# Kernel tuning notes

Measured on AMD Instinct MI355X. Metric: run time of the kernel, lower is better.

## Reference

```python
import jax, jax.numpy as jnp
import numpy as np
from jax.scipy.linalg import cholesky, solve_triangular

SIGMA2 = 0.001   # likelihood.variance (fixed in source)
JITTER = 1e-5


def hankel(v, L):
    # Direct windowed gather; math-identical to the one-hot matmul in the source.
    Nv, Dv = v.shape
    idx = jnp.arange(Nv - L + 1)[:, None] + jnp.arange(L)[None, :]  # [Nv-L+1, L]
    return v[idx].reshape(Nv - L + 1, L * Dv)


def _sqdist(A, B):
    # ||a-b||^2, clipped for numerical safety
    d = jnp.sum(A * A, 1)[:, None] + jnp.sum(B * B, 1)[None, :] - 2.0 * A @ B.T
    return jnp.maximum(d, 0.0)


def _psi_stats(Z, Xmu, Xvar, l2, variance):
    # RBF (ARD) expected-kernel statistics (GPflow conventions).
    N = Xmu.shape[0]
    # psi0: E[k(x,x)] = variance per point, summed over N
    psi0 = jnp.asarray(N, Xmu.dtype) * variance
    # psi1[n,m] = var * prod_q (1+s/l2)^-1/2 * exp(-0.5 (mu-z)^2/(l2+s))
    denom = l2 + Xvar                                        # [N,D]
    logdet1 = -0.5 * jnp.sum(jnp.log1p(Xvar / l2), axis=1)   # [N]
    quad1 = -0.5 * jnp.sum((Xmu[:, None, :] - Z[None, :, :]) ** 2 / denom[:, None, :], axis=2)  # [N,M]
    psi1 = variance * jnp.exp(logdet1[:, None] + quad1)      # [N,M]
    # psi2[n,m,k] = var^2 * prod_q (1+2s/l2)^-1/2
    #   * exp(-(zm-zk)^2/(4 l2) - (mu - (zm+zk)/2)^2 / (2s + l2))
    a = 1.0 / (2.0 * Xvar + l2)                              # [N,D]
    cn = variance ** 2 * jnp.exp(-0.5 * jnp.sum(jnp.log1p(2.0 * Xvar / l2), axis=1))  # [N]
    Zs = Z / (2.0 * jnp.sqrt(l2))
    dZ2 = _sqdist(Zs, Zs)                                    # [M,M], (zm-zk)^2/(4 l2)
    # expand (mu - zbar)^2 * a  without a [N,M,M,D] tensor
    T1 = jnp.sum(a * Xmu * Xmu, axis=1)                      # [N]
    T2 = (a * Xmu) @ Z.T                                     # [N,M]
    T3 = a @ (Z * Z).T                                       # [N,M]
    T4 = jnp.einsum('nq,mq,kq->nmk', a, Z, Z)                # [N,M,M]
    quad2 = (T1[:, None, None] - T2[:, :, None] - T2[:, None, :]
             + 0.25 * (T3[:, :, None] + T3[:, None, :]) + 0.5 * T4)  # [N,M,M]
    psi2 = jnp.sum(cn[:, None, None] * jnp.exp(-dZ2[None, :, :] - quad2), axis=0)  # [M,M]
    return psi0, psi1, psi2


def build_likelihood(X_mean, X_var, Z, lengthscales, variance, Lt):
    N_tot, Q = X_mean.shape
    M = Z.shape[0]
    N = N_tot - Lt
    sigma2 = jnp.asarray(SIGMA2, X_mean.dtype)
    sigma = jnp.sqrt(sigma2)
    l2 = lengthscales ** 2

    X_m = hankel(X_mean[:N_tot - 1], Lt)   # [N, Lt*Q]
    X_v = hankel(X_var[:N_tot - 1], Lt)
    X_mo, X_vo = X_mean[Lt:], X_var[Lt:]   # [N, Q]
    X_mb, X_vb = X_mean[:Lt], X_var[:Lt]   # [Lt, Q]

    Kuu = variance * jnp.exp(-0.5 * _sqdist(Z / lengthscales, Z / lengthscales)) \
          + JITTER * jnp.eye(M, dtype=X_mean.dtype)
    psi0, psi1, psi2 = _psi_stats(Z, X_m, X_v, l2, variance)

    L = cholesky(Kuu, lower=True)
    A = solve_triangular(L, psi1.T, lower=True) / sigma            # [M,N]
    tmp = solve_triangular(L, psi2, lower=True)
    AAT = solve_triangular(L, tmp.T, lower=True) / sigma2          # [M,M]
    B = AAT + jnp.eye(M, dtype=X_mean.dtype)
    LB = cholesky(B, lower=True)
    log_det_B = 2.0 * jnp.sum(jnp.log(jnp.diag(LB)))
    c = solve_triangular(LB, A @ X_mo, lower=True) / sigma         # [M,Q]

    NQ = jnp.asarray(N * Q, X_mean.dtype)
    two_pi = jnp.asarray(2.0 * np.pi, X_mean.dtype)
    ent = 0.5 * jnp.sum(jnp.log(X_vo)) + 0.5 * NQ * jnp.log(two_pi)
    ent2 = -jnp.asarray(Lt * Q, X_mean.dtype) * jnp.log(two_pi) \
           - 0.5 * jnp.sum(X_mb ** 2 + X_vb)

    bound = -0.5 * NQ * jnp.log(two_pi * sigma2)
    bound += -0.5 / sigma2 * (jnp.sum(X_vo) + jnp.sum(X_mo ** 2))
    bound += -0.5 * Q * (psi0 / sigma2 - jnp.trace(AAT))
    bound += -0.5 * Q * log_det_B
    bound += 0.5 * jnp.sum(c ** 2)
    bound += ent + ent2
    return bound


def setup_inputs() -> dict:
    key = jax.random.key(0)
    k1, k2, k3 = jax.random.split(key, 3)
    N, Q, Lt, M = 4096, 4, 8, 128
    D = Lt * Q
    X_mean = jax.random.normal(k1, (N + Lt, Q), dtype=jnp.float32)
    X_var = jax.random.uniform(k2, (N + Lt, Q), dtype=jnp.float32, minval=0.1, maxval=1.0)
    Z = jax.random.normal(k3, (M, D), dtype=jnp.float32)
    lengthscales = 2.0 * jnp.ones((D,), dtype=jnp.float32)
    variance = jnp.asarray(1.0, dtype=jnp.float32)
    return {"X_mean": X_mean, "X_var": X_var, "Z": Z,
            "lengthscales": lengthscales, "variance": variance, "Lt": Lt}


def reference(X_mean, X_var, Z, lengthscales, variance, Lt):
    return build_likelihood(X_mean, X_var, Z, lengthscales, variance, Lt)
```

## Files before the change

kernel.cpp:

```cpp
#include <hip/hip_runtime.h>

#define NN   4096
#define NQ   (NN*4)
#define QQ   4
#define LTT  8
#define DD   32
#define MM   128
#define SIG2 0.001f
#define JIT  1e-5f
#define LOG2E 1.4426950408889634f

typedef _Float16 half8 __attribute__((ext_vector_type(8)));
typedef float    f32x4 __attribute__((ext_vector_type(4)));

__device__ __forceinline__ float fexp2(float x) { return exp2f(x); }

__device__ __forceinline__ float rlane(float v, int l) {
    return __uint_as_float(__builtin_amdgcn_readlane(__float_as_uint(v), l));
}

__global__ __launch_bounds__(256) void prepstatic_kernel(
    const float* __restrict__ Xm, const float* __restrict__ Xv,
    const float* __restrict__ Zg, const float* __restrict__ ls,
    const float* __restrict__ varp,
    float4* __restrict__ pk4, _Float16* __restrict__ bh,
    float* __restrict__ L1p, float* __restrict__ bbp, float* __restrict__ sumsP,
    float* __restrict__ Kuu, float* __restrict__ sp, _Float16* __restrict__ Zh,
    float* __restrict__ Yg, float* __restrict__ scalars, int* __restrict__ cnt)
{
    int b = blockIdx.x, tid = threadIdx.x;
    if (b < 16) {
        __shared__ float ra[256], rb[256], rc[256];
        int n = b*256 + tid;
        float var = varp[0];
        float slog2 = 0.f, slog1 = 0.f, T1 = 0.f, c0 = 0.f;
        #pragma unroll 8
        for (int q = 0; q < DD; ++q) {
            float xm = Xm[n*QQ + q];
            float xv = Xv[n*QQ + q];
            float l  = ls[q];
            float l2 = l*l;
            float a    = 1.0f / (2.0f*xv + l2);
            float dinv = 1.0f / (l2 + xv);
            float4 v;
            v.x = LOG2E * a * xm;
            v.y = LOG2E * (-0.25f * a);
            v.z = dinv;
            v.w = -2.0f * dinv * xm;
            pk4[n*DD + q] = v;
            bh[n*DD + q] = (_Float16)(0.5f * LOG2E * (1.0f/l2 - a));
            slog2 += log1pf(2.0f*xv/l2);
            slog1 += log1pf(xv/l2);
            T1    += a*xm*xm;
            c0    += dinv*xm*xm;
        }
        L1p[n] = 0.5f * LOG2E * (2.0f*logf(var) - 0.5f*slog2 - T1);
        bbp[n] = logf(var) - 0.5f*slog1 - 0.5f*c0;
        float s1 = 0.f, s2 = 0.f, s3 = 0.f;
        #pragma unroll
        for (int c = 0; c < QQ; ++c) {
            float mo = Xm[(n+LTT)*QQ + c];
            float vo = Xv[(n+LTT)*QQ + c];
            s1 += vo + mo*mo;
            s2 += logf(vo);
        }
        if (n < LTT) {
            #pragma unroll
            for (int c = 0; c < QQ; ++c) {
                float mb = Xm[n*QQ+c], vb = Xv[n*QQ+c];
                s3 += mb*mb + vb;
            }
        }
        ra[tid]=s1; rb[tid]=s2; rc[tid]=s3;
        __syncthreads();
        for (int s = 128; s; s >>= 1) {
            if (tid < s) { ra[tid]+=ra[tid+s]; rb[tid]+=rb[tid+s]; rc[tid]+=rc[tid+s]; }
            __syncthreads();
        }
        if (tid == 0) { sumsP[b*3+0]=ra[0]; sumsP[b*3+1]=rb[0]; sumsP[b*3+2]=rc[0]; }
    } else if (b < 80) {
        int idx = (b-16)*256 + tid;
        int i = idx >> 7, j = idx & 127;
        float var = varp[0];
        float s = 0.f;
        for (int q = 0; q < DD; ++q) {
            float l = ls[q];
            float d = (Zg[i*DD+q] - Zg[j*DD+q]) / l;
            s += d*d;
        }
        float v = var * __expf(-0.5f*s);
        if (i == j) v += JIT;
        Kuu[idx] = v;
    } else {
        if (tid < MM) {
            float s = 0.f;
            for (int q = 0; q < DD; ++q) {
                float l = ls[q]; float z = Zg[tid*DD+q];
                s += z*z / (4.0f*l*l);
            }
            sp[tid] = LOG2E * s;
        }
        for (int e = tid; e < MM*DD; e += 256) Zh[e] = (_Float16)Zg[e];
        for (int e = tid; e < 512; e += 256) Yg[e] = 0.f;
        if (tid < 8) scalars[tid] = 0.f;
        if (tid == 0) *cnt = 0;
    }
}

__device__ __forceinline__ void dev_chol(float* mat, int tid)
{
    int wv = tid >> 6, ln = tid & 63;
    for (int p = 0; p < 8; ++p) {
        int base = p*16;
        if (wv == 0) {
            int r0 = base + ln, r1 = r0 + 64;
            bool h0 = r0 < 128, h1 = r1 < 128;
            float a0[16], a1[16];
            #pragma unroll
            for (int c = 0; c < 16; ++c) {
                a0[c] = h0 ? mat[r0*132 + base + c] : 0.f;
                a1[c] = h1 ? mat[r1*132 + base + c] : 0.f;
            }
            #pragma unroll
            for (int kk = 0; kk < 16; ++kk) {
                float d   = rlane(a0[kk], kk);
                float rdk = rsqrtf(d);
                float sq  = d * rdk;
                a0[kk] = (ln == kk) ? sq : a0[kk] * rdk;
                a1[kk] *= rdk;
                #pragma unroll
                for (int j = kk+1; j < 16; ++j) {
                    float ljv = rlane(a0[kk], j);
                    a0[j] = fmaf(-a0[kk], ljv, a0[j]);
                    a1[j] = fmaf(-a1[kk], ljv, a1[j]);
                }
            }
            #pragma unroll
            for (int c = 0; c < 16; ++c) {
                if (h0) mat[r0*132 + base + c] = a0[c];
                if (h1) mat[r1*132 + base + c] = a1[c];
            }
        }
        __syncthreads();
        int S = 112 - base;
        if (S > 0) {
            int T = S >> 2, nb = base + 16;
            int nT = (T*(T+1)) >> 1;
            for (int t = tid; t < nT; t += 256) {
                int ti = (int)(0.5f*(sqrtf(8.f*(float)t + 1.f) - 1.f));
                if ((ti+1)*(ti+2)/2 <= t) ++ti;
                else if (ti*(ti+1)/2 > t) --ti;
                int tj = t - ((ti*(ti+1))>>1);
                int i0 = nb + ti*4, j0 = nb + tj*4;
                float ac[4][4];
                #pragma unroll
                for (int r = 0; r < 4; ++r)
                    #pragma unroll
                    for (int s = 0; s < 4; ++s) ac[r][s] = mat[(i0+r)*132 + j0 + s];
                #pragma unroll
                for (int c4 = 0; c4 < 4; ++c4) {
                    float4 av[4], bv[4];
                    #pragma unroll
                    for (int r = 0; r < 4; ++r) {
                        av[r] = *(const float4*)&mat[(i0+r)*132 + base + c4*4];
                        bv[r] = *(const float4*)&mat[(j0+r)*132 + base + c4*4];
                    }
                    #pragma unroll
                    for (int r = 0; r < 4; ++r)
                        #pragma unroll
                        for (int s = 0; s < 4; ++s)
                            ac[r][s] -= av[r].x*bv[s].x + av[r].y*bv[s].y
                                      + av[r].z*bv[s].z + av[r].w*bv[s].w;
                }
                #pragma unroll
                for (int r = 0; r < 4; ++r)
                    #pragma unroll
                    for (int s = 0; s < 4; ++s) mat[(i0+r)*132 + j0 + s] = ac[r][s];
            }
        }
        __syncthreads();
    }
}

__device__ __forceinline__ void dev_dinv(const float* mat, float* dinvb, int tid)
{
    int wv = tid >> 6, ln = tid & 63;
    if (ln < 16) {
        int c = ln;
        for (int bd = wv; bd < 8; bd += 4) {
            int base = bd*16;
            float x[16];
            #pragma unroll
            for (int i = 0; i < 16; ++i) {
                float dii = mat[(base+i)*132 + base + i];
                float s = 0.f;
                #pragma unroll
                for (int j = 0; j < i; ++j) s += mat[(base+i)*132 + base + j] * x[j];
                float v;
                if (i < c) v = 0.f;
                else if (i == c) v = 1.0f / dii;
                else v = -s / dii;
                x[i] = v;
            }
            #pragma unroll
            for (int i = 0; i < 16; ++i) dinvb[bd*256 + i*16 + c] = x[i];
        }
    }
    __syncthreads();
}

template<int C>
__device__ __forceinline__ void dev_solve(const float* mat, const float* dinvb,
                                          float* tmp, float* rhs, int tid)
{
    const int AT = 16*C;
    int r = tid / C, cc = tid % C;
    for (int bi = 0; bi < 8; ++bi) {
        float acc = 0.f;
        if (tid < AT) {
            acc = rhs[(bi*16+r)*C + cc];
            for (int bk = 0; bk < bi; ++bk) {
                #pragma unroll
                for (int kk = 0; kk < 16; ++kk)
                    acc -= mat[(bi*16+r)*132 + bk*16+kk] * rhs[(bk*16+kk)*C + cc];
            }
        }
        __syncthreads();
        if (tid < AT) tmp[r*C + cc] = acc;
        __syncthreads();
        if (tid < AT) {
            float w = 0.f;
            #pragma unroll
            for (int kk = 0; kk < 16; ++kk)
                w += dinvb[bi*256 + r*16 + kk] * tmp[kk*C + cc];
            rhs[(bi*16+r)*C + cc] = w;
        }
        __syncthreads();
    }
}

template<int C>
__device__ __forceinline__ void dev_bsolve(const float* mat, const float* dinvb,
                                           float* tmp, float* rhs, int tid)
{
    const int AT = 16*C;
    int r = tid / C, cc = tid % C;
    for (int bi = 7; bi >= 0; --bi) {
        float acc = 0.f;
        if (tid < AT) {
            acc = rhs[(bi*16+r)*C + cc];
            for (int bj = bi+1; bj < 8; ++bj) {
                #pragma unroll
                for (int kk = 0; kk < 16; ++kk)
                    acc -= mat[(bj*16+kk)*132 + bi*16 + r] * rhs[(bj*16+kk)*C + cc];
            }
        }
        __syncthreads();
        if (tid < AT) tmp[r*C + cc] = acc;
        __syncthreads();
        if (tid < AT) {
            float w = 0.f;
            #pragma unroll
            for (int kk = 0; kk < 16; ++kk)
                w += dinvb[bi*256 + kk*16 + r] * tmp[kk*C + cc];
            rhs[(bi*16+r)*C + cc] = w;
        }
        __syncthreads();
    }
}

__global__ __launch_bounds__(256) void k1chol_kernel(
    const float* __restrict__ Xm, const float* __restrict__ Zg,
    const float4* __restrict__ pk4, const float* __restrict__ L1p,
    const float* __restrict__ bbp, const float* __restrict__ sp,
    float* __restrict__ r_g, float* __restrict__ Yg, float* __restrict__ psi2,
    const float* __restrict__ Kuu, float* __restrict__ Lg,
    float* __restrict__ Dinvg, float* __restrict__ scalars)
{
    __shared__ float shm[19200];
    int tid = threadIdx.x;
    if (blockIdx.x < 256) {
        float* Zl    = shm;
        float* yredl = shm + 4224;
        { int e = blockIdx.x*64 + tid; if (tid < 64) psi2[e] = 0.f; }
        for (int e = tid; e < MM*DD; e += 256)
            Zl[(e>>5)*33 + (e&31)] = Zg[e];
        __syncthreads();
        int m = tid & 127, half = tid >> 7;
        float zr[DD];
        #pragma unroll
        for (int q = 0; q < DD; ++q) zr[q] = Zl[m*33 + q];
        float sm = sp[m];
        float y0=0.f, y1=0.f, y2=0.f, y3=0.f;
        int n0 = blockIdx.x*16 + half*8;
        for (int i = 0; i < 8; ++i) {
            int n = n0 + i;
            float L1n = L1p[n], bbn = bbp[n];
            const float4* pkn = pk4 + n*DD;
            float racc = 0.f, q1 = 0.f;
            #pragma unroll
            for (int q = 0; q < DD; ++q) {
                float4 v = pkn[q];
                float z = zr[q];
                racc = fmaf(v.x, z, racc);
                racc = fmaf(v.y, z*z, racc);
                float t = fmaf(v.z, z, v.w);
                q1 = fmaf(t, z, q1);
            }
            r_g[n*MM + m] = L1n + racc - sm;
            float p1 = __expf(fmaf(-0.5f, q1, bbn));
            float4 xo = *(const float4*)(Xm + (LTT+n)*QQ);
            y0 = fmaf(p1, xo.x, y0); y1 = fmaf(p1, xo.y, y1);
            y2 = fmaf(p1, xo.z, y2); y3 = fmaf(p1, xo.w, y3);
        }
        if (half == 0) {
            yredl[m*4+0]=y0; yredl[m*4+1]=y1; yredl[m*4+2]=y2; yredl[m*4+3]=y3;
        }
        __syncthreads();
        if (half == 1) {
            yredl[m*4+0]+=y0; yredl[m*4+1]+=y1; yredl[m*4+2]+=y2; yredl[m*4+3]+=y3;
        }
        __syncthreads();
        for (int e = tid; e < 512; e += 256) atomicAdd(&Yg[e], yredl[e]);
    } else {
        float* mat   = shm;
        float* dinvb = shm + 16896;
        float* red   = shm + 18944;
        for (int e = tid; e < 16384; e += 256) mat[(e>>7)*132 + (e&127)] = Kuu[e];
        __syncthreads();
        dev_chol(mat, tid);
        float ld = (tid < 128) ? logf(mat[tid*132 + tid]) : 0.f;
        red[tid] = ld; __syncthreads();
        for (int s = 128; s; s >>= 1) { if (tid < s) red[tid] += red[tid+s]; __syncthreads(); }
        if (tid == 0) scalars[0] = red[0];
        dev_dinv(mat, dinvb, tid);
        for (int e = tid; e < 16384; e += 256) Lg[e] = mat[(e>>7)*132 + (e&127)];
        for (int e = tid; e < 2048; e += 256) Dinvg[e] = dinvb[e];
    }
}

__global__ __launch_bounds__(256) void psi2_kernel(
    const _Float16* __restrict__ Zh, const float* __restrict__ r_g,
    const _Float16* __restrict__ bh, float* __restrict__ psi2)
{
    __shared__ float pacc[4][64][4];
    int tid = threadIdx.x;
    int w = tid >> 6, l = tid & 63, lm = l & 15, lg = l >> 4;
    int b = blockIdx.x;
    int nq = b / 36, t = b - nq*36;
    int kt = (int)(0.5f*(sqrtf(8.f*(float)t + 1.f) - 1.f));
    if ((kt+1)*(kt+2)/2 <= t) ++kt;
    else if (kt*(kt+1)/2 > t) --kt;
    int mt = t - ((kt*(kt+1))>>1);

    half8 Bf = ((const half8*)Zh)[(kt*16 + lm)*4 + lg];
    half8 Zm = ((const half8*)Zh)[(mt*16 + lm)*4 + lg];
    f32x4 z4; z4[0]=0.f; z4[1]=0.f; z4[2]=0.f; z4[3]=0.f;
    f32x4 acc0 = z4, acc1 = z4;
    int n0g = nq*128 + w*32;
    const float* rbase = r_g + (size_t)n0g*MM;
    const half8* bbase = (const half8*)bh + (size_t)n0g*4;
    for (int i = 0; i < 32; i += 2) {
        half8 bf0 = bbase[i*4 + lg];
        half8 bf1 = bbase[i*4 + 4 + lg];
        const float* rn0 = rbase + i*MM;
        f32x4 rm0 = *(const f32x4*)(rn0 + mt*16 + lg*4);
        f32x4 rm1 = *(const f32x4*)(rn0 + MM + mt*16 + lg*4);
        float rk0 = rn0[kt*16 + lm];
        float rk1 = rn0[MM + kt*16 + lm];
        half8 A0 = Zm * bf0;
        half8 A1 = Zm * bf1;
        f32x4 p0 = __builtin_amdgcn_mfma_f32_16x16x32_f16(A0, Bf, z4, 0, 0, 0);
        f32x4 p1 = __builtin_amdgcn_mfma_f32_16x16x32_f16(A1, Bf, z4, 0, 0, 0);
        acc0[0] += fexp2(p0[0] + rm0[0] + rk0);
        acc0[1] += fexp2(p0[1] + rm0[1] + rk0);
        acc0[2] += fexp2(p0[2] + rm0[2] + rk0);
        acc0[3] += fexp2(p0[3] + rm0[3] + rk0);
        acc1[0] += fexp2(p1[0] + rm1[0] + rk1);
        acc1[1] += fexp2(p1[1] + rm1[1] + rk1);
        acc1[2] += fexp2(p1[2] + rm1[2] + rk1);
        acc1[3] += fexp2(p1[3] + rm1[3] + rk1);
    }
    f32x4 acc;
    acc[0]=acc0[0]+acc1[0]; acc[1]=acc0[1]+acc1[1];
    acc[2]=acc0[2]+acc1[2]; acc[3]=acc0[3]+acc1[3];
    #pragma unroll
    for (int j = 0; j < 4; ++j) pacc[w][l][j] = acc[j];
    __syncthreads();
    {
        int ll = tid >> 2, j = tid & 3;
        float s = pacc[0][ll][j] + pacc[1][ll][j] + pacc[2][ll][j] + pacc[3][ll][j];
        int row = mt*16 + (ll >> 4)*4 + j;
        int col = kt*16 + (ll & 15);
        atomicAdd(&psi2[row*MM + col], s);
        if (mt != kt) atomicAdd(&psi2[col*MM + row], s);
    }
}

__global__ __launch_bounds__(256) void cholG_kernel(
    const float* __restrict__ Kuu, const float* __restrict__ psi2,
    const float* __restrict__ Yg, const float* __restrict__ Lg,
    const float* __restrict__ Dinvg, const float* __restrict__ varp,
    const float* __restrict__ sumsP,
    float* __restrict__ scalars, int* __restrict__ cnt, float* __restrict__ out)
{
    __shared__ float mat[128*132];
    __shared__ float dinvb[8*256];
    __shared__ float rhs[128*8];
    __shared__ float tmp[128];
    __shared__ float red[256];
    int tid = threadIdx.x;
    if (blockIdx.x == 0) {
        for (int e = tid; e < 16384; e += 256)
            mat[(e>>7)*132 + (e&127)] = Kuu[e] + (1.0f/SIG2)*psi2[e];
        __syncthreads();
        dev_chol(mat, tid);
        float ld = (tid < 128) ? logf(mat[tid*132 + tid]) : 0.f;
        red[tid] = ld; __syncthreads();
        for (int s = 128; s; s >>= 1) { if (tid < s) red[tid] += red[tid+s]; __syncthreads(); }
        if (tid == 0) scalars[1] = red[0];
        dev_dinv(mat, dinvb, tid);
        if (tid < 256) { rhs[tid] = Yg[tid]; rhs[tid+256] = Yg[tid+256]; }
        __syncthreads();
        dev_solve<4>(mat, dinvb, tmp, rhs, tid);
        float c2 = rhs[tid]*rhs[tid] + rhs[tid+256]*rhs[tid+256];
        red[tid] = c2; __syncthreads();
        for (int s = 128; s; s >>= 1) { if (tid < s) red[tid] += red[tid+s]; __syncthreads(); }
        if (tid == 0) scalars[2] = red[0];
    } else {
        int c0 = (blockIdx.x - 1) * 8;
        for (int e = tid; e < 16384; e += 256) mat[(e>>7)*132 + (e&127)] = Lg[e];
        for (int e = tid; e < 2048; e += 256) dinvb[e] = Dinvg[e];
        for (int e = tid; e < 1024; e += 256) {
            int i = e >> 3, cc = e & 7;
            rhs[e] = (i == c0 + cc) ? 1.0f : 0.0f;
        }
        __syncthreads();
        dev_bsolve<8>(mat, dinvb, tmp, rhs, tid);
        int i = tid & 127, cp = tid >> 7;
        float vv0=0.f, vv1=0.f, vv2=0.f, vv3=0.f;
        for (int j = 0; j < 128; ++j) {
            float pj = psi2[j*MM + i];
            vv0 = fmaf(pj, rhs[j*8 + cp*4 + 0], vv0);
            vv1 = fmaf(pj, rhs[j*8 + cp*4 + 1], vv1);
            vv2 = fmaf(pj, rhs[j*8 + cp*4 + 2], vv2);
            vv3 = fmaf(pj, rhs[j*8 + cp*4 + 3], vv3);
        }
        float part = rhs[i*8 + cp*4 + 0]*vv0 + rhs[i*8 + cp*4 + 1]*vv1
                   + rhs[i*8 + cp*4 + 2]*vv2 + rhs[i*8 + cp*4 + 3]*vv3;
        red[tid] = part; __syncthreads();
        for (int s = 128; s; s >>= 1) { if (tid < s) red[tid] += red[tid+s]; __syncthreads(); }
        if (tid == 0) atomicAdd(&scalars[3], red[0]);
    }
    if (tid == 0) {
        __threadfence();
        int old = atomicAdd(cnt, 1);
        if (old == 16) {
            float ldK  = scalars[0];
            float ldG  = atomicAdd(&scalars[1], 0.0f);
            float c2s  = atomicAdd(&scalars[2], 0.0f);
            float trr  = atomicAdd(&scalars[3], 0.0f);
            float s1=0.f, s2=0.f, s3=0.f;
            for (int b2 = 0; b2 < 16; ++b2) {
                s1 += sumsP[b2*3+0]; s2 += sumsP[b2*3+1]; s3 += sumsP[b2*3+2];
            }
            float var = varp[0];
            float trAAT   = trr / SIG2;
            float logdetB = 2.0f * (ldG - ldK);
            float sumc2   = c2s / (SIG2*SIG2);
            float psi0    = (float)NN * var;
            const float LOG2PI = 1.837877066409345f;
            float NQf = (float)NQ;
            float bound = -0.5f*NQf*(LOG2PI + logf(SIG2));
            bound += -0.5f/SIG2 * s1;
            bound += -0.5f*(float)QQ*(psi0/SIG2 - trAAT);
            bound += -0.5f*(float)QQ*logdetB;
            bound += 0.5f*sumc2;
            bound += 0.5f*s2 + 0.5f*NQf*LOG2PI;
            bound += -(float)(LTT*QQ)*LOG2PI - 0.5f*s3;
            out[0] = bound;
        }
    }
}

extern "C" void kernel_launch(void* const* d_in, const int* in_sizes, int n_in,
                              void* d_out, int out_size, void* d_ws, size_t ws_size,
                              hipStream_t stream)
{
    (void)in_sizes; (void)n_in; (void)out_size; (void)ws_size;
    const float* Xm   = (const float*)d_in[0];
    const float* Xv   = (const float*)d_in[1];
    const float* Zg   = (const float*)d_in[2];
    const float* ls   = (const float*)d_in[3];
    const float* varp = (const float*)d_in[4];

    float* p = (float*)d_ws;
    float4*   pk4   = (float4*)p;       p += NN*DD*4;
    float*    r_g   = p;                p += NN*MM;
    _Float16* bh    = (_Float16*)p;     p += NN*DD/2;
    _Float16* Zh    = (_Float16*)p;     p += MM*DD/2;
    float*    L1p   = p;                p += NN;
    float*    bbp   = p;                p += NN;
    float*    sp    = p;                p += MM;
    float*    Kuu   = p;                p += MM*MM;
    float*    Lg    = p;                p += MM*MM;
    float*    Dinvg = p;                p += 2048;
    float*    psi2  = p;                p += MM*MM;
    float*    Yg    = p;                p += 512;
    float*    sumsP = p;                p += 64;
    float*    scalars = p;              p += 8;
    int*      cnt   = (int*)p;          p += 4;

    prepstatic_kernel<<<81, 256, 0, stream>>>(Xm, Xv, Zg, ls, varp,
                                              pk4, bh, L1p, bbp, sumsP, Kuu, sp, Zh,
                                              Yg, scalars, cnt);
    k1chol_kernel<<<257, 256, 0, stream>>>(Xm, Zg, pk4, L1p, bbp, sp, r_g, Yg, psi2,
                                           Kuu, Lg, Dinvg, scalars);
    psi2_kernel<<<1152, 256, 0, stream>>>(Zh, r_g, bh, psi2);
    cholG_kernel<<<17, 256, 0, stream>>>(Kuu, psi2, Yg, Lg, Dinvg, varp, sumsP,
                                         scalars, cnt, (float*)d_out);
}
```

Baseline: 187.6 us.

## Move Kuu Cholesky into psi2 launch and widen serial solver blocks to 512 threads

```diff
diff --git a/kernel.cpp b/kernel.cpp
--- a/kernel.cpp
+++ b/kernel.cpp
@@ -107,6 +107,58 @@
     }
 }
 
+__global__ __launch_bounds__(256) void k1_kernel(
+    const float* __restrict__ Xm, const float* __restrict__ Zg,
+    const float4* __restrict__ pk4, const float* __restrict__ L1p,
+    const float* __restrict__ bbp, const float* __restrict__ sp,
+    float* __restrict__ r_g, float* __restrict__ Yg, float* __restrict__ psi2)
+{
+    __shared__ float Zl[MM*33];
+    __shared__ float yredl[MM*QQ];
+    int tid = threadIdx.x;
+    { int e = blockIdx.x*64 + tid; if (tid < 64) psi2[e] = 0.f; }
+    for (int e = tid; e < MM*DD; e += 256)
+        Zl[(e>>5)*33 + (e&31)] = Zg[e];
+    __syncthreads();
+    int m = tid & 127, half = tid >> 7;
+    float zr[DD];
+    #pragma unroll
+    for (int q = 0; q < DD; ++q) zr[q] = Zl[m*33 + q];
+    float sm = sp[m];
+    float y0=0.f, y1=0.f, y2=0.f, y3=0.f;
+    int n0 = blockIdx.x*16 + half*8;
+    for (int i = 0; i < 8; ++i) {
+        int n = n0 + i;
+        float L1n = L1p[n], bbn = bbp[n];
+        const float4* pkn = pk4 + n*DD;
+        float racc = 0.f, q1 = 0.f;
+        #pragma unroll
+        for (int q = 0; q < DD; ++q) {
+            float4 v = pkn[q];
+            float z = zr[q];
+            racc = fmaf(v.x, z, racc);
+            racc = fmaf(v.y, z*z, racc);
+            float t = fmaf(v.z, z, v.w);
+            q1 = fmaf(t, z, q1);
+        }
+        r_g[n*MM + m] = L1n + racc - sm;
+        float p1 = __expf(fmaf(-0.5f, q1, bbn));
+        float4 xo = *(const float4*)(Xm + (LTT+n)*QQ);
+        y0 = fmaf(p1, xo.x, y0); y1 = fmaf(p1, xo.y, y1);
+        y2 = fmaf(p1, xo.z, y2); y3 = fmaf(p1, xo.w, y3);
+    }
+    if (half == 0) {
+        yredl[m*4+0]=y0; yredl[m*4+1]=y1; yredl[m*4+2]=y2; yredl[m*4+3]=y3;
+    }
+    __syncthreads();
+    if (half == 1) {
+        yredl[m*4+0]+=y0; yredl[m*4+1]+=y1; yredl[m*4+2]+=y2; yredl[m*4+3]+=y3;
+    }
+    __syncthreads();
+    for (int e = tid; e < 512; e += 256) atomicAdd(&Yg[e], yredl[e]);
+}
+
+template<int NT>
 __device__ __forceinline__ void dev_chol(float* mat, int tid)
 {
     int wv = tid >> 6, ln = tid & 63;
@@ -146,7 +198,7 @@
         if (S > 0) {
             int T = S >> 2, nb = base + 16;
             int nT = (T*(T+1)) >> 1;
-            for (int t = tid; t < nT; t += 256) {
+            for (int t = tid; t < nT; t += NT) {
                 int ti = (int)(0.5f*(sqrtf(8.f*(float)t + 1.f) - 1.f));
                 if ((ti+1)*(ti+2)/2 <= t) ++ti;
                 else if (ti*(ti+1)/2 > t) --ti;
@@ -182,12 +234,13 @@
     }
 }
 
+template<int NT>
 __device__ __forceinline__ void dev_dinv(const float* mat, float* dinvb, int tid)
 {
     int wv = tid >> 6, ln = tid & 63;
     if (ln < 16) {
         int c = ln;
-        for (int bd = wv; bd < 8; bd += 4) {
+        for (int bd = wv; bd < 8; bd += NT/64) {
             int base = bd*16;
             float x[16];
             #pragma unroll
@@ -207,36 +260,6 @@
         }
     }
     __syncthreads();
-}
-
-template<int C>
-__device__ __forceinline__ void dev_solve(const float* mat, const float* dinvb,
-                                          float* tmp, float* rhs, int tid)
-{
-    const int AT = 16*C;
-    int r = tid / C, cc = tid % C;
-    for (int bi = 0; bi < 8; ++bi) {
-        float acc = 0.f;
-        if (tid < AT) {
-            acc = rhs[(bi*16+r)*C + cc];
-            for (int bk = 0; bk < bi; ++bk) {
-                #pragma unroll
-                for (int kk = 0; kk < 16; ++kk)
-                    acc -= mat[(bi*16+r)*132 + bk*16+kk] * rhs[(bk*16+kk)*C + cc];
-            }
-        }
-        __syncthreads();
-        if (tid < AT) tmp[r*C + cc] = acc;
-        __syncthreads();
-        if (tid < AT) {
-            float w = 0.f;
-            #pragma unroll
-            for (int kk = 0; kk < 16; ++kk)
-                w += dinvb[bi*256 + r*16 + kk] * tmp[kk*C + cc];
-            rhs[(bi*16+r)*C + cc] = w;
-        }
-        __syncthreads();
-    }
 }
 
 template<int C>
@@ -269,135 +292,83 @@
     }
 }
 
-__global__ __launch_bounds__(256) void k1chol_kernel(
-    const float* __restrict__ Xm, const float* __restrict__ Zg,
-    const float4* __restrict__ pk4, const float* __restrict__ L1p,
-    const float* __restrict__ bbp, const float* __restrict__ sp,
-    float* __restrict__ r_g, float* __restrict__ Yg, float* __restrict__ psi2,
+__global__ __launch_bounds__(512) void psi2chol_kernel(
+    const _Float16* __restrict__ Zh, const float* __restrict__ r_g,
+    const _Float16* __restrict__ bh, float* __restrict__ psi2,
     const float* __restrict__ Kuu, float* __restrict__ Lg,
     float* __restrict__ Dinvg, float* __restrict__ scalars)
 {
-    __shared__ float shm[19200];
+    __shared__ float shm[19456];
     int tid = threadIdx.x;
-    if (blockIdx.x < 256) {
-        float* Zl    = shm;
-        float* yredl = shm + 4224;
-        { int e = blockIdx.x*64 + tid; if (tid < 64) psi2[e] = 0.f; }
-        for (int e = tid; e < MM*DD; e += 256)
-            Zl[(e>>5)*33 + (e&31)] = Zg[e];
-        __syncthreads();
-        int m = tid & 127, half = tid >> 7;
-        float zr[DD];
-        #pragma unroll
-        for (int q = 0; q < DD; ++q) zr[q] = Zl[m*33 + q];
-        float sm = sp[m];
-        float y0=0.f, y1=0.f, y2=0.f, y3=0.f;
-        int n0 = blockIdx.x*16 + half*8;
-        for (int i = 0; i < 8; ++i) {
-            int n = n0 + i;
-            float L1n = L1p[n], bbn = bbp[n];
-            const float4* pkn = pk4 + n*DD;
-            float racc = 0.f, q1 = 0.f;
-            #pragma unroll
-            for (int q = 0; q < DD; ++q) {
-                float4 v = pkn[q];
-                float z = zr[q];
-                racc = fmaf(v.x, z, racc);
-                racc = fmaf(v.y, z*z, racc);
-                float t = fmaf(v.z, z, v.w);
-                q1 = fmaf(t, z, q1);
-            }
-            r_g[n*MM + m] = L1n + racc - sm;
-            float p1 = __expf(fmaf(-0.5f, q1, bbn));
-            float4 xo = *(const float4*)(Xm + (LTT+n)*QQ);
-            y0 = fmaf(p1, xo.x, y0); y1 = fmaf(p1, xo.y, y1);
-            y2 = fmaf(p1, xo.z, y2); y3 = fmaf(p1, xo.w, y3);
-        }
-        if (half == 0) {
-            yredl[m*4+0]=y0; yredl[m*4+1]=y1; yredl[m*4+2]=y2; yredl[m*4+3]=y3;
-        }
-        __syncthreads();
-        if (half == 1) {
-            yredl[m*4+0]+=y0; yredl[m*4+1]+=y1; yredl[m*4+2]+=y2; yredl[m*4+3]+=y3;
-        }
-        __syncthreads();
-        for (int e = tid; e < 512; e += 256) atomicAdd(&Yg[e], yredl[e]);
-    } else {
+    if (blockIdx.x == 0) {
         float* mat   = shm;
         float* dinvb = shm + 16896;
         float* red   = shm + 18944;
-        for (int e = tid; e < 16384; e += 256) mat[(e>>7)*132 + (e&127)] = Kuu[e];
-        __syncthreads();
-        dev_chol(mat, tid);
-        float ld = (tid < 128) ? logf(mat[tid*132 + tid]) : 0.f;
-        red[tid] = ld; __syncthreads();
-        for (int s = 128; s; s >>= 1) { if (tid < s) red[tid] += red[tid+s]; __syncthreads(); }
+        for (int e = tid; e < 16384; e += 512) mat[(e>>7)*132 + (e&127)] = Kuu[e];
+        __syncthreads();
+        dev_chol<512>(mat, tid);
+        red[tid] = (tid < 128) ? logf(mat[tid*132 + tid]) : 0.f;
+        __syncthreads();
+        for (int s = 256; s; s >>= 1) { if (tid < s) red[tid] += red[tid+s]; __syncthreads(); }
         if (tid == 0) scalars[0] = red[0];
-        dev_dinv(mat, dinvb, tid);
-        for (int e = tid; e < 16384; e += 256) Lg[e] = mat[(e>>7)*132 + (e&127)];
-        for (int e = tid; e < 2048; e += 256) Dinvg[e] = dinvb[e];
-    }
-}
-
-__global__ __launch_bounds__(256) void psi2_kernel(
-    const _Float16* __restrict__ Zh, const float* __restrict__ r_g,
-    const _Float16* __restrict__ bh, float* __restrict__ psi2)
-{
-    __shared__ float pacc[4][64][4];
-    int tid = threadIdx.x;
-    int w = tid >> 6, l = tid & 63, lm = l & 15, lg = l >> 4;
-    int b = blockIdx.x;
-    int nq = b / 36, t = b - nq*36;
-    int kt = (int)(0.5f*(sqrtf(8.f*(float)t + 1.f) - 1.f));
-    if ((kt+1)*(kt+2)/2 <= t) ++kt;
-    else if (kt*(kt+1)/2 > t) --kt;
-    int mt = t - ((kt*(kt+1))>>1);
-
-    half8 Bf = ((const half8*)Zh)[(kt*16 + lm)*4 + lg];
-    half8 Zm = ((const half8*)Zh)[(mt*16 + lm)*4 + lg];
-    f32x4 z4; z4[0]=0.f; z4[1]=0.f; z4[2]=0.f; z4[3]=0.f;
-    f32x4 acc0 = z4, acc1 = z4;
-    int n0g = nq*128 + w*32;
-    const float* rbase = r_g + (size_t)n0g*MM;
-    const half8* bbase = (const half8*)bh + (size_t)n0g*4;
-    for (int i = 0; i < 32; i += 2) {
-        half8 bf0 = bbase[i*4 + lg];
-        half8 bf1 = bbase[i*4 + 4 + lg];
-        const float* rn0 = rbase + i*MM;
-        f32x4 rm0 = *(const f32x4*)(rn0 + mt*16 + lg*4);
-        f32x4 rm1 = *(const f32x4*)(rn0 + MM + mt*16 + lg*4);
-        float rk0 = rn0[kt*16 + lm];
-        float rk1 = rn0[MM + kt*16 + lm];
-        half8 A0 = Zm * bf0;
-        half8 A1 = Zm * bf1;
-        f32x4 p0 = __builtin_amdgcn_mfma_f32_16x16x32_f16(A0, Bf, z4, 0, 0, 0);
-        f32x4 p1 = __builtin_amdgcn_mfma_f32_16x16x32_f16(A1, Bf, z4, 0, 0, 0);
-        acc0[0] += fexp2(p0[0] + rm0[0] + rk0);
-        acc0[1] += fexp2(p0[1] + rm0[1] + rk0);
-        acc0[2] += fexp2(p0[2] + rm0[2] + rk0);
-        acc0[3] += fexp2(p0[3] + rm0[3] + rk0);
-        acc1[0] += fexp2(p1[0] + rm1[0] + rk1);
-        acc1[1] += fexp2(p1[1] + rm1[1] + rk1);
-        acc1[2] += fexp2(p1[2] + rm1[2] + rk1);
-        acc1[3] += fexp2(p1[3] + rm1[3] + rk1);
-    }
-    f32x4 acc;
-    acc[0]=acc0[0]+acc1[0]; acc[1]=acc0[1]+acc1[1];
-    acc[2]=acc0[2]+acc1[2]; acc[3]=acc0[3]+acc1[3];
-    #pragma unroll
-    for (int j = 0; j < 4; ++j) pacc[w][l][j] = acc[j];
-    __syncthreads();
-    {
-        int ll = tid >> 2, j = tid & 3;
-        float s = pacc[0][ll][j] + pacc[1][ll][j] + pacc[2][ll][j] + pacc[3][ll][j];
-        int row = mt*16 + (ll >> 4)*4 + j;
-        int col = kt*16 + (ll & 15);
-        atomicAdd(&psi2[row*MM + col], s);
-        if (mt != kt) atomicAdd(&psi2[col*MM + row], s);
-    }
-}
-
-__global__ __launch_bounds__(256) void cholG_kernel(
+        dev_dinv<512>(mat, dinvb, tid);
+        for (int e = tid; e < 16384; e += 512) Lg[e] = mat[(e>>7)*132 + (e&127)];
+        for (int e = tid; e < 2048; e += 512) Dinvg[e] = dinvb[e];
+    } else {
+        float (*pacc)[64][4] = (float(*)[64][4])shm;
+        int w = tid >> 6, l = tid & 63, lm = l & 15, lg = l >> 4;
+        int b = blockIdx.x - 1;
+        int t = b % 36, nq = b / 36;
+        int kt = (int)(0.5f*(sqrtf(8.f*(float)t + 1.f) - 1.f));
+        if ((kt+1)*(kt+2)/2 <= t) ++kt;
+        else if (kt*(kt+1)/2 > t) --kt;
+        int mt = t - ((kt*(kt+1))>>1);
+
+        half8 Bf = ((const half8*)Zh)[(kt*16 + lm)*4 + lg];
+        half8 Zm = ((const half8*)Zh)[(mt*16 + lm)*4 + lg];
+        f32x4 z4; z4[0]=0.f; z4[1]=0.f; z4[2]=0.f; z4[3]=0.f;
+        f32x4 acc0 = z4, acc1 = z4;
+        int n0g = nq*128 + w*16;
+        const float* rbase = r_g + (size_t)n0g*MM;
+        const half8* bbase = (const half8*)bh + (size_t)n0g*4;
+        for (int i = 0; i < 16; i += 2) {
+            half8 bf0 = bbase[i*4 + lg];
+            half8 bf1 = bbase[i*4 + 4 + lg];
+            const float* rn0 = rbase + i*MM;
+            f32x4 rm0 = *(const f32x4*)(rn0 + mt*16 + lg*4);
+            f32x4 rm1 = *(const f32x4*)(rn0 + MM + mt*16 + lg*4);
+            float rk0 = rn0[kt*16 + lm];
+            float rk1 = rn0[MM + kt*16 + lm];
+            half8 A0 = Zm * bf0;
+            half8 A1 = Zm * bf1;
+            f32x4 p0 = __builtin_amdgcn_mfma_f32_16x16x32_f16(A0, Bf, z4, 0, 0, 0);
+            f32x4 p1 = __builtin_amdgcn_mfma_f32_16x16x32_f16(A1, Bf, z4, 0, 0, 0);
+            acc0[0] += fexp2(p0[0] + rm0[0] + rk0);
+            acc0[1] += fexp2(p0[1] + rm0[1] + rk0);
+            acc0[2] += fexp2(p0[2] + rm0[2] + rk0);
+            acc0[3] += fexp2(p0[3] + rm0[3] + rk0);
+            acc1[0] += fexp2(p1[0] + rm1[0] + rk1);
+            acc1[1] += fexp2(p1[1] + rm1[1] + rk1);
+            acc1[2] += fexp2(p1[2] + rm1[2] + rk1);
+            acc1[3] += fexp2(p1[3] + rm1[3] + rk1);
+        }
+        #pragma unroll
+        for (int j = 0; j < 4; ++j) pacc[w][l][j] = acc0[j] + acc1[j];
+        __syncthreads();
+        if (tid < 256) {
+            int ll = tid >> 2, j = tid & 3;
+            float s = 0.f;
+            #pragma unroll
+            for (int ww = 0; ww < 8; ++ww) s += pacc[ww][ll][j];
+            int row = mt*16 + (ll >> 4)*4 + j;
+            int col = kt*16 + (ll & 15);
+            atomicAdd(&psi2[row*MM + col], s);
+            if (mt != kt) atomicAdd(&psi2[col*MM + row], s);
+        }
+    }
+}
+
+__global__ __launch_bounds__(512) void cholG_kernel(
     const float* __restrict__ Kuu, const float* __restrict__ psi2,
     const float* __restrict__ Yg, const float* __restrict__ Lg,
     const float* __restrict__ Dinvg, const float* __restrict__ varp,
@@ -408,38 +379,61 @@
     __shared__ float dinvb[8*256];
     __shared__ float rhs[128*8];
     __shared__ float tmp[128];
-    __shared__ float red[256];
+    __shared__ float red[512];
     int tid = threadIdx.x;
     if (blockIdx.x == 0) {
-        for (int e = tid; e < 16384; e += 256)
+        for (int e = tid; e < 16384; e += 512)
             mat[(e>>7)*132 + (e&127)] = Kuu[e] + (1.0f/SIG2)*psi2[e];
         __syncthreads();
-        dev_chol(mat, tid);
-        float ld = (tid < 128) ? logf(mat[tid*132 + tid]) : 0.f;
-        red[tid] = ld; __syncthreads();
-        for (int s = 128; s; s >>= 1) { if (tid < s) red[tid] += red[tid+s]; __syncthreads(); }
+        dev_chol<512>(mat, tid);
+        red[tid] = (tid < 128) ? logf(mat[tid*132 + tid]) : 0.f;
+        __syncthreads();
+        for (int s = 256; s; s >>= 1) { if (tid < s) red[tid] += red[tid+s]; __syncthreads(); }
         if (tid == 0) scalars[1] = red[0];
-        dev_dinv(mat, dinvb, tid);
-        if (tid < 256) { rhs[tid] = Yg[tid]; rhs[tid+256] = Yg[tid+256]; }
-        __syncthreads();
-        dev_solve<4>(mat, dinvb, tmp, rhs, tid);
-        float c2 = rhs[tid]*rhs[tid] + rhs[tid+256]*rhs[tid+256];
-        red[tid] = c2; __syncthreads();
-        for (int s = 128; s; s >>= 1) { if (tid < s) red[tid] += red[tid+s]; __syncthreads(); }
+        dev_dinv<512>(mat, dinvb, tid);
+        rhs[tid & 511] = Yg[tid & 511];
+        __syncthreads();
+        if (tid < 64) {
+            int r = tid >> 2, cc = tid & 3;
+            for (int bi = 0; bi < 8; ++bi) {
+                float a0 = rhs[(bi*16+r)*4 + cc], a1 = 0.f, a2 = 0.f, a3 = 0.f;
+                for (int bk = 0; bk < bi; ++bk) {
+                    const float* mrow = &mat[(bi*16+r)*132 + bk*16];
+                    const float* rb   = &rhs[bk*64 + cc];
+                    #pragma unroll
+                    for (int kk = 0; kk < 16; kk += 4) {
+                        a0 = fmaf(-mrow[kk+0], rb[(kk+0)*4], a0);
+                        a1 = fmaf(-mrow[kk+1], rb[(kk+1)*4], a1);
+                        a2 = fmaf(-mrow[kk+2], rb[(kk+2)*4], a2);
+                        a3 = fmaf(-mrow[kk+3], rb[(kk+3)*4], a3);
+                    }
+                }
+                float acc = (a0+a1)+(a2+a3);
+                float w = 0.f;
+                #pragma unroll
+                for (int kk = 0; kk < 16; ++kk)
+                    w += dinvb[bi*256 + r*16 + kk] * __shfl(acc, kk*4 + cc, 64);
+                rhs[(bi*16+r)*4 + cc] = w;
+            }
+        }
+        __syncthreads();
+        { float v = rhs[tid & 511]; red[tid] = v*v; }
+        __syncthreads();
+        for (int s = 256; s; s >>= 1) { if (tid < s) red[tid] += red[tid+s]; __syncthreads(); }
         if (tid == 0) scalars[2] = red[0];
     } else {
         int c0 = (blockIdx.x - 1) * 8;
-        for (int e = tid; e < 16384; e += 256) mat[(e>>7)*132 + (e&127)] = Lg[e];
-        for (int e = tid; e < 2048; e += 256) dinvb[e] = Dinvg[e];
-        for (int e = tid; e < 1024; e += 256) {
+        for (int e = tid; e < 16384; e += 512) mat[(e>>7)*132 + (e&127)] = Lg[e];
+        for (int e = tid; e < 2048; e += 512) dinvb[e] = Dinvg[e];
+        for (int e = tid; e < 1024; e += 512) {
             int i = e >> 3, cc = e & 7;
             rhs[e] = (i == c0 + cc) ? 1.0f : 0.0f;
         }
         __syncthreads();
         dev_bsolve<8>(mat, dinvb, tmp, rhs, tid);
-        int i = tid & 127, cp = tid >> 7;
+        int i = tid & 127, cp = (tid >> 7) & 1, jh = tid >> 8;
         float vv0=0.f, vv1=0.f, vv2=0.f, vv3=0.f;
-        for (int j = 0; j < 128; ++j) {
+        for (int j = jh*64; j < jh*64 + 64; ++j) {
             float pj = psi2[j*MM + i];
             vv0 = fmaf(pj, rhs[j*8 + cp*4 + 0], vv0);
             vv1 = fmaf(pj, rhs[j*8 + cp*4 + 1], vv1);
@@ -448,8 +442,9 @@
         }
         float part = rhs[i*8 + cp*4 + 0]*vv0 + rhs[i*8 + cp*4 + 1]*vv1
                    + rhs[i*8 + cp*4 + 2]*vv2 + rhs[i*8 + cp*4 + 3]*vv3;
-        red[tid] = part; __syncthreads();
-        for (int s = 128; s; s >>= 1) { if (tid < s) red[tid] += red[tid+s]; __syncthreads(); }
+        red[tid] = part;
+        __syncthreads();
+        for (int s = 256; s; s >>= 1) { if (tid < s) red[tid] += red[tid+s]; __syncthreads(); }
         if (tid == 0) atomicAdd(&scalars[3], red[0]);
     }
     if (tid == 0) {
@@ -514,9 +509,8 @@
     prepstatic_kernel<<<81, 256, 0, stream>>>(Xm, Xv, Zg, ls, varp,
                                               pk4, bh, L1p, bbp, sumsP, Kuu, sp, Zh,
                                               Yg, scalars, cnt);
-    k1chol_kernel<<<257, 256, 0, stream>>>(Xm, Zg, pk4, L1p, bbp, sp, r_g, Yg, psi2,
-                                           Kuu, Lg, Dinvg, scalars);
-    psi2_kernel<<<1152, 256, 0, stream>>>(Zh, r_g, bh, psi2);
-    cholG_kernel<<<17, 256, 0, stream>>>(Kuu, psi2, Yg, Lg, Dinvg, varp, sumsP,
+    k1_kernel<<<256, 256, 0, stream>>>(Xm, Zg, pk4, L1p, bbp, sp, r_g, Yg, psi2);
+    psi2chol_kernel<<<1153, 512, 0, stream>>>(Zh, r_g, bh, psi2, Kuu, Lg, Dinvg, scalars);
+    cholG_kernel<<<17, 512, 0, stream>>>(Kuu, psi2, Yg, Lg, Dinvg, varp, sumsP,
                                          scalars, cnt, (float*)d_out);
 }
```

New measurement: 177.5 us. -5.3%, faster.
